# Kernel optimization log

Hardware: AMD Instinct MI355X
Metric: run time of the kernel (lower is better)

The kernel has to match this reference:

```python
import jax, jax.numpy as jnp
import numpy as np

# SMPL kinematic tree parents (joint 0 is root)
SMPL_PARENTS = [-1, 0, 0, 0, 1, 2, 3, 4, 5, 6, 7, 8, 9, 9, 9, 12, 13, 14, 16, 17, 18, 19, 20, 21]
NUM_JOINTS = 24


def _rodrigues(axisang):
    # axisang: (B, J, 3) -> (B, J, 3, 3), matching th_posemap_axisang's eps handling
    angle = jnp.linalg.norm(axisang + 1e-8, axis=-1, keepdims=True)  # (B,J,1)
    axis = axisang / angle
    a = angle[..., None]                      # (B,J,1,1)
    c, s = jnp.cos(a), jnp.sin(a)
    x, y, z = axis[..., 0], axis[..., 1], axis[..., 2]
    zero = jnp.zeros_like(x)
    # skew-symmetric cross-product matrix K
    K = jnp.stack([
        jnp.stack([zero, -z, y], axis=-1),
        jnp.stack([z, zero, -x], axis=-1),
        jnp.stack([-y, x, zero], axis=-1),
    ], axis=-2)                               # (B,J,3,3)
    outer = axis[..., :, None] * axis[..., None, :]
    eye = jnp.eye(3, dtype=axisang.dtype)
    return c * eye + (1.0 - c) * outer + s * K


def setup_inputs() -> dict:
    key = jax.random.key(0)
    k1, k2, k3 = jax.random.split(key, 3)
    B, N = 16, 100000
    normals = jax.random.normal(k1, (B, 3, N), dtype=jnp.float32)
    pose = jax.random.normal(k2, (B, 72), dtype=jnp.float32)
    skinning_weights = jax.random.uniform(k3, (B, NUM_JOINTS, N), dtype=jnp.float32)
    return {"normals": normals, "pose": pose, "skinning_weights": skinning_weights}


def reference(normals, pose, skinning_weights):
    B = pose.shape[0]
    rots = _rodrigues(pose.reshape(B, NUM_JOINTS, 3))  # (B,24,3,3)
    # sequential kinematic-chain composition over the fixed 24-joint tree
    results = [rots[:, 0]]
    for i in range(1, NUM_JOINTS):
        results.append(jnp.matmul(results[SMPL_PARENTS[i]], rots[:, i]))
    th_results2 = jnp.stack(results, axis=-1)          # (B,3,3,24)
    # skinning: (B,9,24) @ (B,24,N) -> (B,3,3,N)
    n_T = jnp.einsum('bijk,bkn->bijn', th_results2, skinning_weights)
    # rotate normals: sum over local axis j of n_T[b,i,j,n] * normals[b,j,n]
    n_verts = jnp.einsum('bijn,bjn->bin', n_T, normals)  # (B,3,N)
    return n_verts
```

## Files before the change

### kernel.cpp

```cpp
#include <hip/hip_runtime.h>

#define NUM_JOINTS 24

__device__ __constant__ int d_parents[NUM_JOINTS] = {
    -1, 0, 0, 0, 1, 2, 3, 4, 5, 6, 7, 8, 9, 9, 9, 12, 13, 14, 16, 17, 18, 19, 20, 21
};

__global__ __launch_bounds__(64) void chain_kernel(const float* __restrict__ pose,
                                                   float* __restrict__ R) {
    __shared__ float L[NUM_JOINTS][9];
    __shared__ float G[NUM_JOINTS][9];
    const int b = blockIdx.x;
    const int tid = threadIdx.x;

    if (tid < NUM_JOINTS) {
        float x = pose[b * 72 + tid * 3 + 0];
        float y = pose[b * 72 + tid * 3 + 1];
        float z = pose[b * 72 + tid * 3 + 2];
        float ax = x + 1e-8f, ay = y + 1e-8f, az = z + 1e-8f;
        float angle = sqrtf(ax * ax + ay * ay + az * az);
        float inv = 1.0f / angle;
        float ux = x * inv, uy = y * inv, uz = z * inv;
        float c = cosf(angle), s = sinf(angle), t = 1.0f - c;
        L[tid][0] = c + t * ux * ux;
        L[tid][1] = t * ux * uy - s * uz;
        L[tid][2] = t * ux * uz + s * uy;
        L[tid][3] = t * uy * ux + s * uz;
        L[tid][4] = c + t * uy * uy;
        L[tid][5] = t * uy * uz - s * ux;
        L[tid][6] = t * uz * ux - s * uy;
        L[tid][7] = t * uz * uy + s * ux;
        L[tid][8] = c + t * uz * uz;
    }
    __syncthreads();

    if (tid == 0) {
        #pragma unroll
        for (int e = 0; e < 9; e++) G[0][e] = L[0][e];
        for (int i = 1; i < NUM_JOINTS; i++) {
            int p = d_parents[i];
            #pragma unroll
            for (int r = 0; r < 3; r++) {
                #pragma unroll
                for (int cc = 0; cc < 3; cc++) {
                    G[i][r * 3 + cc] = G[p][r * 3 + 0] * L[i][0 * 3 + cc]
                                     + G[p][r * 3 + 1] * L[i][1 * 3 + cc]
                                     + G[p][r * 3 + 2] * L[i][2 * 3 + cc];
                }
            }
        }
    }
    __syncthreads();

    for (int idx = tid; idx < NUM_JOINTS * 9; idx += blockDim.x) {
        R[b * NUM_JOINTS * 9 + idx] = G[idx / 9][idx % 9];
    }
}

__device__ __forceinline__ float4 fma4(float4 a, float s, float4 c) {
    return make_float4(fmaf(a.x, s, c.x), fmaf(a.y, s, c.y),
                       fmaf(a.z, s, c.z), fmaf(a.w, s, c.w));
}

__global__ __launch_bounds__(256) void skin_kernel(const float* __restrict__ normals,
                                                   const float* __restrict__ weights,
                                                   const float* __restrict__ R,
                                                   float* __restrict__ out,
                                                   int N) {
    __shared__ float4 Rl[NUM_JOINTS][3];

    const int b = blockIdx.y;
    const int tid = threadIdx.x;

    {
        float* Rf = (float*)Rl;
        const float* Rg = R + b * NUM_JOINTS * 9;
        if (tid < NUM_JOINTS * 9) {
            Rf[(tid / 9) * 12 + (tid % 9)] = Rg[tid];
        }
    }
    __syncthreads();

    const int q8 = blockIdx.x * blockDim.x + tid;
    const int n8 = N >> 3;
    const int nf4 = N >> 2;

    const float4* __restrict__ Wb = (const float4*)(weights + (size_t)b * NUM_JOINTS * N);
    const float4* __restrict__ Nb = (const float4*)(normals + (size_t)b * 3 * N);
    float4* __restrict__ Ob = (float4*)(out + (size_t)b * 3 * N);

    if (q8 < n8) {
        float4 m0[9], m1[9];
        #pragma unroll
        for (int e = 0; e < 9; e++) {
            m0[e] = make_float4(0.f, 0.f, 0.f, 0.f);
            m1[e] = make_float4(0.f, 0.f, 0.f, 0.f);
        }

        #pragma unroll 4
        for (int k = 0; k < NUM_JOINTS; k++) {
            float4 w0 = Wb[(size_t)k * nf4 + (q8 << 1)];
            float4 w1 = Wb[(size_t)k * nf4 + (q8 << 1) + 1];
            float4 r0 = Rl[k][0];
            float4 r1 = Rl[k][1];
            float4 r2 = Rl[k][2];
            m0[0] = fma4(w0, r0.x, m0[0]); m1[0] = fma4(w1, r0.x, m1[0]);
            m0[1] = fma4(w0, r0.y, m0[1]); m1[1] = fma4(w1, r0.y, m1[1]);
            m0[2] = fma4(w0, r0.z, m0[2]); m1[2] = fma4(w1, r0.z, m1[2]);
            m0[3] = fma4(w0, r0.w, m0[3]); m1[3] = fma4(w1, r0.w, m1[3]);
            m0[4] = fma4(w0, r1.x, m0[4]); m1[4] = fma4(w1, r1.x, m1[4]);
            m0[5] = fma4(w0, r1.y, m0[5]); m1[5] = fma4(w1, r1.y, m1[5]);
            m0[6] = fma4(w0, r1.z, m0[6]); m1[6] = fma4(w1, r1.z, m1[6]);
            m0[7] = fma4(w0, r1.w, m0[7]); m1[7] = fma4(w1, r1.w, m1[7]);
            m0[8] = fma4(w0, r2.x, m0[8]); m1[8] = fma4(w1, r2.x, m1[8]);
        }

        float4 nx0 = Nb[(size_t)0 * nf4 + (q8 << 1)], nx1 = Nb[(size_t)0 * nf4 + (q8 << 1) + 1];
        float4 ny0 = Nb[(size_t)1 * nf4 + (q8 << 1)], ny1 = Nb[(size_t)1 * nf4 + (q8 << 1) + 1];
        float4 nz0 = Nb[(size_t)2 * nf4 + (q8 << 1)], nz1 = Nb[(size_t)2 * nf4 + (q8 << 1) + 1];

        #pragma unroll
        for (int i = 0; i < 3; i++) {
            float4 o0, o1;
            o0.x = fmaf(m0[3*i].x, nx0.x, fmaf(m0[3*i+1].x, ny0.x, m0[3*i+2].x * nz0.x));
            o0.y = fmaf(m0[3*i].y, nx0.y, fmaf(m0[3*i+1].y, ny0.y, m0[3*i+2].y * nz0.y));
            o0.z = fmaf(m0[3*i].z, nx0.z, fmaf(m0[3*i+1].z, ny0.z, m0[3*i+2].z * nz0.z));
            o0.w = fmaf(m0[3*i].w, nx0.w, fmaf(m0[3*i+1].w, ny0.w, m0[3*i+2].w * nz0.w));
            o1.x = fmaf(m1[3*i].x, nx1.x, fmaf(m1[3*i+1].x, ny1.x, m1[3*i+2].x * nz1.x));
            o1.y = fmaf(m1[3*i].y, nx1.y, fmaf(m1[3*i+1].y, ny1.y, m1[3*i+2].y * nz1.y));
            o1.z = fmaf(m1[3*i].z, nx1.z, fmaf(m1[3*i+1].z, ny1.z, m1[3*i+2].z * nz1.z));
            o1.w = fmaf(m1[3*i].w, nx1.w, fmaf(m1[3*i+1].w, ny1.w, m1[3*i+2].w * nz1.w));
            Ob[(size_t)i * nf4 + (q8 << 1)] = o0;
            Ob[(size_t)i * nf4 + (q8 << 1) + 1] = o1;
        }
    } else if (q8 == n8 && (N & 7) != 0) {
        const float* Rf = (const float*)Rl;
        for (int n = n8 * 8; n < N; n++) {
            float m[9];
            #pragma unroll
            for (int e = 0; e < 9; e++) m[e] = 0.f;
            for (int k = 0; k < NUM_JOINTS; k++) {
                float w = weights[(size_t)b * NUM_JOINTS * N + (size_t)k * N + n];
                #pragma unroll
                for (int e = 0; e < 9; e++) m[e] = fmaf(w, Rf[k * 12 + e], m[e]);
            }
            float vx = normals[(size_t)b * 3 * N + 0 * N + n];
            float vy = normals[(size_t)b * 3 * N + 1 * N + n];
            float vz = normals[(size_t)b * 3 * N + 2 * N + n];
            for (int i = 0; i < 3; i++) {
                out[(size_t)b * 3 * N + (size_t)i * N + n] =
                    fmaf(m[3 * i], vx, fmaf(m[3 * i + 1], vy, m[3 * i + 2] * vz));
            }
        }
    }
}

extern "C" void kernel_launch(void* const* d_in, const int* in_sizes, int n_in,
                              void* d_out, int out_size, void* d_ws, size_t ws_size,
                              hipStream_t stream) {
    const float* normals = (const float*)d_in[0];
    const float* pose = (const float*)d_in[1];
    const float* weights = (const float*)d_in[2];
    float* out = (float*)d_out;
    float* R = (float*)d_ws;

    const int B = in_sizes[1] / 72;
    const int N = in_sizes[0] / (3 * B);

    chain_kernel<<<dim3(B), dim3(64), 0, stream>>>(pose, R);

    const int n8 = (N + 7) >> 3;
    const int gx = (n8 + 255) / 256;
    skin_kernel<<<dim3(gx, B), dim3(256), 0, stream>>>(normals, weights, R, out, N);
}
```

Measured before the change: 249.6 us.

## Fuse kinematic chain into skinning kernel with parallel per-joint chain products

Removes the separate chain kernel and its global workspace round-trip. Each skinning block now recomputes the Rodrigues rotations and the global joint rotations itself. Each of the 24 threads multiplies its own precomputed ancestor path instead of one thread walking the tree serially. Weight, normal and output accesses also switch to nontemporal loads and stores to reduce cache pollution on the streaming data. The cost is redundant per-block chain work (trig plus up to 8 small matmuls) before streaming begins.

Result: faster. 231.3 us (-7.3%).

```diff
diff --git a/kernel.cpp b/kernel.cpp
--- a/kernel.cpp
+++ b/kernel.cpp
@@ -2,15 +2,52 @@
 
 #define NUM_JOINTS 24
 
-__device__ __constant__ int d_parents[NUM_JOINTS] = {
-    -1, 0, 0, 0, 1, 2, 3, 4, 5, 6, 7, 8, 9, 9, 9, 12, 13, 14, 16, 17, 18, 19, 20, 21
+typedef float fvec4 __attribute__((ext_vector_type(4)));
+
+__device__ __constant__ int d_chain[NUM_JOINTS][9] = {
+    {0,-1,-1,-1,-1,-1,-1,-1,-1},
+    {0,1,-1,-1,-1,-1,-1,-1,-1},
+    {0,2,-1,-1,-1,-1,-1,-1,-1},
+    {0,3,-1,-1,-1,-1,-1,-1,-1},
+    {0,1,4,-1,-1,-1,-1,-1,-1},
+    {0,2,5,-1,-1,-1,-1,-1,-1},
+    {0,3,6,-1,-1,-1,-1,-1,-1},
+    {0,1,4,7,-1,-1,-1,-1,-1},
+    {0,2,5,8,-1,-1,-1,-1,-1},
+    {0,3,6,9,-1,-1,-1,-1,-1},
+    {0,1,4,7,10,-1,-1,-1,-1},
+    {0,2,5,8,11,-1,-1,-1,-1},
+    {0,3,6,9,12,-1,-1,-1,-1},
+    {0,3,6,9,13,-1,-1,-1,-1},
+    {0,3,6,9,14,-1,-1,-1,-1},
+    {0,3,6,9,12,15,-1,-1,-1},
+    {0,3,6,9,13,16,-1,-1,-1},
+    {0,3,6,9,14,17,-1,-1,-1},
+    {0,3,6,9,13,16,18,-1,-1},
+    {0,3,6,9,14,17,19,-1,-1},
+    {0,3,6,9,13,16,18,20,-1},
+    {0,3,6,9,14,17,19,21,-1},
+    {0,3,6,9,13,16,18,20,22},
+    {0,3,6,9,14,17,19,21,23},
 };
 
-__global__ __launch_bounds__(64) void chain_kernel(const float* __restrict__ pose,
-                                                   float* __restrict__ R) {
+__device__ __forceinline__ fvec4 fma4(fvec4 a, float s, fvec4 c) {
+    fvec4 r;
+    r.x = fmaf(a.x, s, c.x); r.y = fmaf(a.y, s, c.y);
+    r.z = fmaf(a.z, s, c.z); r.w = fmaf(a.w, s, c.w);
+    return r;
+}
+
+__global__ __launch_bounds__(256) void skin_fused_kernel(
+    const float* __restrict__ normals,
+    const float* __restrict__ pose,
+    const float* __restrict__ weights,
+    float* __restrict__ out,
+    int N) {
     __shared__ float L[NUM_JOINTS][9];
-    __shared__ float G[NUM_JOINTS][9];
-    const int b = blockIdx.x;
+    __shared__ fvec4 Rl[NUM_JOINTS][3];
+
+    const int b = blockIdx.y;
     const int tid = threadIdx.x;
 
     if (tid < NUM_JOINTS) {
@@ -34,50 +71,32 @@
     }
     __syncthreads();
 
-    if (tid == 0) {
+    if (tid < NUM_JOINTS) {
+        float G[9];
+        int j0 = d_chain[tid][0];
         #pragma unroll
-        for (int e = 0; e < 9; e++) G[0][e] = L[0][e];
-        for (int i = 1; i < NUM_JOINTS; i++) {
-            int p = d_parents[i];
-            #pragma unroll
-            for (int r = 0; r < 3; r++) {
+        for (int e = 0; e < 9; e++) G[e] = L[j0][e];
+        #pragma unroll
+        for (int d = 1; d < 9; d++) {
+            int j = d_chain[tid][d];
+            if (j >= 0) {
+                float T[9];
                 #pragma unroll
-                for (int cc = 0; cc < 3; cc++) {
-                    G[i][r * 3 + cc] = G[p][r * 3 + 0] * L[i][0 * 3 + cc]
-                                     + G[p][r * 3 + 1] * L[i][1 * 3 + cc]
-                                     + G[p][r * 3 + 2] * L[i][2 * 3 + cc];
+                for (int r = 0; r < 3; r++) {
+                    #pragma unroll
+                    for (int cc = 0; cc < 3; cc++) {
+                        T[r * 3 + cc] = G[r * 3 + 0] * L[j][0 * 3 + cc]
+                                      + G[r * 3 + 1] * L[j][1 * 3 + cc]
+                                      + G[r * 3 + 2] * L[j][2 * 3 + cc];
+                    }
                 }
+                #pragma unroll
+                for (int e = 0; e < 9; e++) G[e] = T[e];
             }
         }
-    }
-    __syncthreads();
-
-    for (int idx = tid; idx < NUM_JOINTS * 9; idx += blockDim.x) {
-        R[b * NUM_JOINTS * 9 + idx] = G[idx / 9][idx % 9];
-    }
-}
-
-__device__ __forceinline__ float4 fma4(float4 a, float s, float4 c) {
-    return make_float4(fmaf(a.x, s, c.x), fmaf(a.y, s, c.y),
-                       fmaf(a.z, s, c.z), fmaf(a.w, s, c.w));
-}
-
-__global__ __launch_bounds__(256) void skin_kernel(const float* __restrict__ normals,
-                                                   const float* __restrict__ weights,
-                                                   const float* __restrict__ R,
-                                                   float* __restrict__ out,
-                                                   int N) {
-    __shared__ float4 Rl[NUM_JOINTS][3];
-
-    const int b = blockIdx.y;
-    const int tid = threadIdx.x;
-
-    {
         float* Rf = (float*)Rl;
-        const float* Rg = R + b * NUM_JOINTS * 9;
-        if (tid < NUM_JOINTS * 9) {
-            Rf[(tid / 9) * 12 + (tid % 9)] = Rg[tid];
-        }
+        #pragma unroll
+        for (int e = 0; e < 9; e++) Rf[tid * 12 + e] = G[e];
     }
     __syncthreads();
 
@@ -85,25 +104,25 @@
     const int n8 = N >> 3;
     const int nf4 = N >> 2;
 
-    const float4* __restrict__ Wb = (const float4*)(weights + (size_t)b * NUM_JOINTS * N);
-    const float4* __restrict__ Nb = (const float4*)(normals + (size_t)b * 3 * N);
-    float4* __restrict__ Ob = (float4*)(out + (size_t)b * 3 * N);
+    const fvec4* __restrict__ Wb = (const fvec4*)(weights + (size_t)b * NUM_JOINTS * N);
+    const fvec4* __restrict__ Nb = (const fvec4*)(normals + (size_t)b * 3 * N);
+    fvec4* __restrict__ Ob = (fvec4*)(out + (size_t)b * 3 * N);
 
     if (q8 < n8) {
-        float4 m0[9], m1[9];
+        fvec4 m0[9], m1[9];
         #pragma unroll
         for (int e = 0; e < 9; e++) {
-            m0[e] = make_float4(0.f, 0.f, 0.f, 0.f);
-            m1[e] = make_float4(0.f, 0.f, 0.f, 0.f);
+            m0[e] = (fvec4)(0.f);
+            m1[e] = (fvec4)(0.f);
         }
 
         #pragma unroll 4
         for (int k = 0; k < NUM_JOINTS; k++) {
-            float4 w0 = Wb[(size_t)k * nf4 + (q8 << 1)];
-            float4 w1 = Wb[(size_t)k * nf4 + (q8 << 1) + 1];
-            float4 r0 = Rl[k][0];
-            float4 r1 = Rl[k][1];
-            float4 r2 = Rl[k][2];
+            fvec4 w0 = __builtin_nontemporal_load(&Wb[(size_t)k * nf4 + (q8 << 1)]);
+            fvec4 w1 = __builtin_nontemporal_load(&Wb[(size_t)k * nf4 + (q8 << 1) + 1]);
+            fvec4 r0 = Rl[k][0];
+            fvec4 r1 = Rl[k][1];
+            fvec4 r2 = Rl[k][2];
             m0[0] = fma4(w0, r0.x, m0[0]); m1[0] = fma4(w1, r0.x, m1[0]);
             m0[1] = fma4(w0, r0.y, m0[1]); m1[1] = fma4(w1, r0.y, m1[1]);
             m0[2] = fma4(w0, r0.z, m0[2]); m1[2] = fma4(w1, r0.z, m1[2]);
@@ -115,13 +134,16 @@
             m0[8] = fma4(w0, r2.x, m0[8]); m1[8] = fma4(w1, r2.x, m1[8]);
         }
 
-        float4 nx0 = Nb[(size_t)0 * nf4 + (q8 << 1)], nx1 = Nb[(size_t)0 * nf4 + (q8 << 1) + 1];
-        float4 ny0 = Nb[(size_t)1 * nf4 + (q8 << 1)], ny1 = Nb[(size_t)1 * nf4 + (q8 << 1) + 1];
-        float4 nz0 = Nb[(size_t)2 * nf4 + (q8 << 1)], nz1 = Nb[(size_t)2 * nf4 + (q8 << 1) + 1];
+        fvec4 nx0 = __builtin_nontemporal_load(&Nb[(size_t)0 * nf4 + (q8 << 1)]);
+        fvec4 nx1 = __builtin_nontemporal_load(&Nb[(size_t)0 * nf4 + (q8 << 1) + 1]);
+        fvec4 ny0 = __builtin_nontemporal_load(&Nb[(size_t)1 * nf4 + (q8 << 1)]);
+        fvec4 ny1 = __builtin_nontemporal_load(&Nb[(size_t)1 * nf4 + (q8 << 1) + 1]);
+        fvec4 nz0 = __builtin_nontemporal_load(&Nb[(size_t)2 * nf4 + (q8 << 1)]);
+        fvec4 nz1 = __builtin_nontemporal_load(&Nb[(size_t)2 * nf4 + (q8 << 1) + 1]);
 
         #pragma unroll
         for (int i = 0; i < 3; i++) {
-            float4 o0, o1;
+            fvec4 o0, o1;
             o0.x = fmaf(m0[3*i].x, nx0.x, fmaf(m0[3*i+1].x, ny0.x, m0[3*i+2].x * nz0.x));
             o0.y = fmaf(m0[3*i].y, nx0.y, fmaf(m0[3*i+1].y, ny0.y, m0[3*i+2].y * nz0.y));
             o0.z = fmaf(m0[3*i].z, nx0.z, fmaf(m0[3*i+1].z, ny0.z, m0[3*i+2].z * nz0.z));
@@ -130,8 +152,8 @@
             o1.y = fmaf(m1[3*i].y, nx1.y, fmaf(m1[3*i+1].y, ny1.y, m1[3*i+2].y * nz1.y));
             o1.z = fmaf(m1[3*i].z, nx1.z, fmaf(m1[3*i+1].z, ny1.z, m1[3*i+2].z * nz1.z));
             o1.w = fmaf(m1[3*i].w, nx1.w, fmaf(m1[3*i+1].w, ny1.w, m1[3*i+2].w * nz1.w));
-            Ob[(size_t)i * nf4 + (q8 << 1)] = o0;
-            Ob[(size_t)i * nf4 + (q8 << 1) + 1] = o1;
+            __builtin_nontemporal_store(o0, &Ob[(size_t)i * nf4 + (q8 << 1)]);
+            __builtin_nontemporal_store(o1, &Ob[(size_t)i * nf4 + (q8 << 1) + 1]);
         }
     } else if (q8 == n8 && (N & 7) != 0) {
         const float* Rf = (const float*)Rl;
@@ -162,14 +184,11 @@
     const float* pose = (const float*)d_in[1];
     const float* weights = (const float*)d_in[2];
     float* out = (float*)d_out;
-    float* R = (float*)d_ws;
 
     const int B = in_sizes[1] / 72;
     const int N = in_sizes[0] / (3 * B);
 
-    chain_kernel<<<dim3(B), dim3(64), 0, stream>>>(pose, R);
-
     const int n8 = (N + 7) >> 3;
     const int gx = (n8 + 255) / 256;
-    skin_kernel<<<dim3(gx, B), dim3(256), 0, stream>>>(normals, weights, R, out, N);
+    skin_fused_kernel<<<dim3(gx, B), dim3(256), 0, stream>>>(normals, pose, weights, out, N);
 }
```
